# Kernel tuning notes

Measured on AMD Instinct MI355X. Metric: run time of the kernel, lower is better.

Reference implementation:

```python
import jax, jax.numpy as jnp
import numpy as np

U1, U2 = 128, 32  # GRU units


def gru(x, kernel, rec_kernel, bias, act, rec_act):
    """Keras GRU with reset_after=True. x: [B,T,F], kernel: [F,3U],
    rec_kernel: [U,3U], bias: [2,3U] (input bias, recurrent bias).
    Gate order is [z, r, h]. Returns (sequence [B,T,U], last state [B,U])."""
    B = x.shape[0]
    U = rec_kernel.shape[0]
    # Precompute the input projection for all timesteps in one big matmul.
    xb = jnp.einsum('btf,fg->btg', x, kernel) + bias[0]  # [B,T,3U]

    def step(h, xt):
        inner = h @ rec_kernel + bias[1]                 # [B,3U]
        xz, xr, xh = jnp.split(xt, 3, axis=-1)
        iz, ir, ih = jnp.split(inner, 3, axis=-1)
        z = rec_act(xz + iz)
        r = rec_act(xr + ir)
        hh = act(xh + r * ih)
        h_new = z * h + (1.0 - z) * hh
        return h_new, h_new

    h0 = jnp.zeros((B, U), x.dtype)
    hT, hs = jax.lax.scan(step, h0, jnp.swapaxes(xb, 0, 1))  # scan over T
    return jnp.swapaxes(hs, 0, 1), hT


def setup_inputs() -> dict:
    key = jax.random.key(0)
    ks = jax.random.split(key, 9)
    B, T, F = 512, 1024, 1
    s = 0.05
    return {
        'x':   jax.random.normal(ks[0], (B, T, F), jnp.float32),
        'k1':  jax.random.normal(ks[1], (F, 3 * U1), jnp.float32) * s,
        'rk1': jax.random.normal(ks[2], (U1, 3 * U1), jnp.float32) * s,
        'b1':  jnp.zeros((2, 3 * U1), jnp.float32),
        'k2':  jax.random.normal(ks[3], (U1, 3 * U2), jnp.float32) * s,
        'rk2': jax.random.normal(ks[4], (U2, 3 * U2), jnp.float32) * s,
        'b2':  jnp.zeros((2, 3 * U2), jnp.float32),
        'wd':  jax.random.normal(ks[5], (U2, 1), jnp.float32) * s,
        'bd':  jnp.zeros((1,), jnp.float32),
    }


def reference(x, k1, rk1, b1, k2, rk2, b2, wd, bd):
    # GRU-1: activation=tanh, recurrent_activation=relu, return_sequences=True
    seq1, _ = gru(x, k1, rk1, b1, jnp.tanh, jax.nn.relu)
    # Dropout(0.5) is identity at inference time.
    # GRU-2: activation=relu, recurrent_activation=sigmoid, return last state
    _, h2 = gru(seq1, k2, rk2, b2, jax.nn.relu, jax.nn.sigmoid)
    return h2 @ wd + bd  # [B,1]
```

## Files before the change

### kernel.cpp

```cpp
#include <hip/hip_runtime.h>
#include <math.h>

#define TT 1024
#define U1 128
#define U2 32
#define NCOL 480
#define NCP 240
#define NUQ 4

typedef float f2 __attribute__((ext_vector_type(2)));

#define PK_LO(acc, w, h) asm("v_pk_fma_f32 %0, %1, %2, %0 op_sel:[0,0,0] op_sel_hi:[1,0,1]" \
                             : "+v"(acc) : "v"(w), "v"(h))
#define PK_HI(acc, w, h) asm("v_pk_fma_f32 %0, %1, %2, %0 op_sel:[0,1,0] op_sel_hi:[1,1,1]" \
                             : "+v"(acc) : "v"(w), "v"(h))

__device__ __forceinline__ float fast_tanh(float v) {
    float e = __expf(2.f * v);
    return 1.f - 2.f / (e + 1.f);
}
__device__ __forceinline__ float fast_sig(float v) {
    return 1.f / (1.f + __expf(-v));
}

__global__ __launch_bounds__(1024)
void gru_stack_kernel(const float* __restrict__ x,
                      const float* __restrict__ k1,
                      const float* __restrict__ rk1,
                      const float* __restrict__ b1,
                      const float* __restrict__ k2,
                      const float* __restrict__ rk2,
                      const float* __restrict__ b2,
                      const float* __restrict__ wd,
                      const float* __restrict__ bd,
                      float* __restrict__ out)
{
    __shared__ __align__(16) float h1s[2][U1];
    __shared__ __align__(16) float h2s[2][U2];
    __shared__ __align__(16) float part1[2][NUQ][NCOL];
    __shared__ __align__(16) float part2[2][96];
    __shared__ __align__(16) float xs[2][TT];

    const int t  = threadIdx.x;
    const int b0 = blockIdx.x * 2;

    if (t < 2 * U1) ((float*)h1s)[t] = 0.f;
    if (t < 2 * U2) ((float*)h2s)[t] = 0.f;
    for (int idx = t; idx < 2 * TT; idx += 1024)
        ((float*)xs)[idx] = x[b0 * TT + idx];

    f2 w2[32];
    const float4* pb0 = nullptr;
    const float4* pb1 = nullptr;
    float2* pd0 = nullptr;
    float2* pd1 = nullptr;
    const bool is_dot = (t < 1008);
    if (t < 960) {
        const int uq = t / NCP, p = t % NCP;
        const int c0 = 2 * p, ub = 32 * uq;
#pragma unroll
        for (int j = 0; j < 32; ++j) {
            const int u = ub + j;
            float vv[2];
#pragma unroll
            for (int r = 0; r < 2; ++r) {
                const int c = c0 + r;
                vv[r] = (c < 384) ? rk1[u * 384 + c] : k2[u * 96 + (c - 384)];
            }
            w2[j].x = vv[0]; w2[j].y = vv[1];
        }
        pb0 = (const float4*)&h1s[0][ub];
        pb1 = (const float4*)&h1s[1][ub];
        pd0 = (float2*)&part1[0][uq][c0];
        pd1 = (float2*)&part1[1][uq][c0];
    } else if (t < 1008) {
        const int q2 = t - 960, c0 = 2 * q2;
#pragma unroll
        for (int j = 0; j < 32; ++j) {
            w2[j].x = rk2[j * 96 + c0 + 0];
            w2[j].y = rk2[j * 96 + c0 + 1];
        }
        pb0 = (const float4*)&h2s[0][0];
        pb1 = (const float4*)&h2s[1][0];
        pd0 = (float2*)&part2[0][c0];
        pd1 = (float2*)&part2[1][c0];
    } else {
#pragma unroll
        for (int j = 0; j < 32; ++j) { w2[j].x = 0.f; w2[j].y = 0.f; }
    }

    const int ju = t & 127, bu = t >> 7;
    float k1z = 0, k1r = 0, k1h = 0, bz = 0, br = 0, bhx = 0, bhr = 0, h_old = 0;
    if (t < 256) {
        k1z = k1[ju]; k1r = k1[128 + ju]; k1h = k1[256 + ju];
        bz  = b1[ju]       + b1[384 + ju];
        br  = b1[128 + ju] + b1[384 + 128 + ju];
        bhx = b1[256 + ju];
        bhr = b1[384 + 256 + ju];
    }
    const int tau = t - 256, j2 = tau & 31, bb2 = tau >> 5;
    float bz2 = 0, br2 = 0, bh2x = 0, bh2r = 0, h2_old = 0;
    if (t >= 256 && t < 320) {
        bz2  = b2[j2]      + b2[96 + j2];
        br2  = b2[32 + j2] + b2[96 + 32 + j2];
        bh2x = b2[64 + j2];
        bh2r = b2[96 + 64 + j2];
    }

    __syncthreads();

    for (int i = 0; i <= TT; ++i) {
        if (is_dot) {
            f2 a0 = {0.f, 0.f};
            f2 a1 = {0.f, 0.f};
#pragma unroll
            for (int k = 0; k < 8; ++k) {
                const float4 h0 = pb0[k];
                const float4 h1 = pb1[k];
                const f2 h0lo = {h0.x, h0.y}, h0hi = {h0.z, h0.w};
                const f2 h1lo = {h1.x, h1.y}, h1hi = {h1.z, h1.w};
                PK_LO(a0, w2[4 * k],     h0lo);
                PK_HI(a0, w2[4 * k + 1], h0lo);
                PK_LO(a0, w2[4 * k + 2], h0hi);
                PK_HI(a0, w2[4 * k + 3], h0hi);
                PK_LO(a1, w2[4 * k],     h1lo);
                PK_HI(a1, w2[4 * k + 1], h1lo);
                PK_LO(a1, w2[4 * k + 2], h1hi);
                PK_HI(a1, w2[4 * k + 3], h1hi);
            }
            *pd0 = make_float2(a0.x, a0.y);
            *pd1 = make_float2(a1.x, a1.y);
        }
        __syncthreads();

        if (t < 256 && i < TT) {
            const float xv = xs[bu][i];
            float iz = part1[bu][0][ju] + part1[bu][1][ju]
                     + part1[bu][2][ju] + part1[bu][3][ju];
            float ir = part1[bu][0][128 + ju] + part1[bu][1][128 + ju]
                     + part1[bu][2][128 + ju] + part1[bu][3][128 + ju];
            float ih = part1[bu][0][256 + ju] + part1[bu][1][256 + ju]
                     + part1[bu][2][256 + ju] + part1[bu][3][256 + ju];
            float z  = fmaxf(fmaf(xv, k1z, bz) + iz, 0.f);
            float r  = fmaxf(fmaf(xv, k1r, br) + ir, 0.f);
            float hh = fast_tanh(fmaf(xv, k1h, bhx) + r * (ih + bhr));
            h_old = fmaf(z, h_old - hh, hh);
            h1s[bu][ju] = h_old;
        } else if (t >= 256 && t < 320 && i >= 1) {
            float xz = part1[bb2][0][384 + j2] + part1[bb2][1][384 + j2]
                     + part1[bb2][2][384 + j2] + part1[bb2][3][384 + j2];
            float xr = part1[bb2][0][416 + j2] + part1[bb2][1][416 + j2]
                     + part1[bb2][2][416 + j2] + part1[bb2][3][416 + j2];
            float xh = part1[bb2][0][448 + j2] + part1[bb2][1][448 + j2]
                     + part1[bb2][2][448 + j2] + part1[bb2][3][448 + j2];
            float iz = part2[bb2][j2];
            float ir = part2[bb2][32 + j2];
            float ih = part2[bb2][64 + j2];
            float z  = fast_sig(xz + iz + bz2);
            float r  = fast_sig(xr + ir + br2);
            float hh = fmaxf(xh + bh2x + r * (ih + bh2r), 0.f);
            h2_old = fmaf(z, h2_old - hh, hh);
            h2s[bb2][j2] = h2_old;
        }
        __syncthreads();
    }

    if (t < 64) {
        const int b = t >> 5, j = t & 31;
        float p = h2s[b][j] * wd[j];
#pragma unroll
        for (int m = 16; m >= 1; m >>= 1) p += __shfl_xor(p, m, 64);
        if (j == 0) out[b0 + b] = p + bd[0];
    }
}

extern "C" void kernel_launch(void* const* d_in, const int* in_sizes, int n_in,
                              void* d_out, int out_size, void* d_ws, size_t ws_size,
                              hipStream_t stream) {
    const float* x   = (const float*)d_in[0];
    const float* k1  = (const float*)d_in[1];
    const float* rk1 = (const float*)d_in[2];
    const float* b1  = (const float*)d_in[3];
    const float* k2  = (const float*)d_in[4];
    const float* rk2 = (const float*)d_in[5];
    const float* b2  = (const float*)d_in[6];
    const float* wd  = (const float*)d_in[7];
    const float* bd  = (const float*)d_in[8];
    float* out = (float*)d_out;

    dim3 grid(256), block(1024);
    hipLaunchKernelGGL(gru_stack_kernel, grid, block, 0, stream,
                       x, k1, rk1, b1, k2, rk2, b2, wd, bd, out);
}
```

Baseline: 1.178 ms.

## Broadcast hidden state via readlane into SGPRs instead of LDS float4 loads

Each wave now loads one hidden-state element per lane from LDS and broadcasts it with v_readlane into scalar registers that feed packed FMAs. This replaces repeated per-thread float4 LDS reads of the shared hidden vector. The thread-to-column mapping is reorganised by wave: the rk2 recurrent dot product is folded into the spare lanes of the fourth wave of each unit quarter, and the gate-update threads are remapped to whole waves. The change adds many readlane instructions and an extra rk2 loop executed by every 'heavy' wave.

```diff
diff --git a/kernel.cpp b/kernel.cpp
--- a/kernel.cpp
+++ b/kernel.cpp
@@ -4,16 +4,14 @@
 #define TT 1024
 #define U1 128
 #define U2 32
-#define NCOL 480
-#define NCP 240
-#define NUQ 4
+#define PCOL 512
 
 typedef float f2 __attribute__((ext_vector_type(2)));
 
-#define PK_LO(acc, w, h) asm("v_pk_fma_f32 %0, %1, %2, %0 op_sel:[0,0,0] op_sel_hi:[1,0,1]" \
-                             : "+v"(acc) : "v"(w), "v"(h))
-#define PK_HI(acc, w, h) asm("v_pk_fma_f32 %0, %1, %2, %0 op_sel:[0,1,0] op_sel_hi:[1,1,1]" \
-                             : "+v"(acc) : "v"(w), "v"(h))
+#define PKS_LO(acc, w, hs) asm("v_pk_fma_f32 %0, %1, %2, %0 op_sel:[0,0,0] op_sel_hi:[1,0,1]" \
+                               : "+v"(acc) : "v"(w), "s"(hs))
+#define PKS_HI(acc, w, hs) asm("v_pk_fma_f32 %0, %1, %2, %0 op_sel:[0,1,0] op_sel_hi:[1,1,1]" \
+                               : "+v"(acc) : "v"(w), "s"(hs))
 
 __device__ __forceinline__ float fast_tanh(float v) {
     float e = __expf(2.f * v);
@@ -21,6 +19,9 @@
 }
 __device__ __forceinline__ float fast_sig(float v) {
     return 1.f / (1.f + __expf(-v));
+}
+__device__ __forceinline__ float rlf(float v, int l) {
+    return __int_as_float(__builtin_amdgcn_readlane(__float_as_int(v), l));
 }
 
 __global__ __launch_bounds__(1024)
@@ -37,70 +38,62 @@
 {
     __shared__ __align__(16) float h1s[2][U1];
     __shared__ __align__(16) float h2s[2][U2];
-    __shared__ __align__(16) float part1[2][NUQ][NCOL];
+    __shared__ __align__(16) float part1[2][4][PCOL];
     __shared__ __align__(16) float part2[2][96];
     __shared__ __align__(16) float xs[2][TT];
 
-    const int t  = threadIdx.x;
-    const int b0 = blockIdx.x * 2;
+    const int t    = threadIdx.x;
+    const int b0   = blockIdx.x * 2;
+    const int w    = t >> 6, lane = t & 63;
+    const int uq   = w >> 2, ub = 32 * uq;
+    const int pi   = ((w & 3) << 6) + lane;
+    const bool heavy = ((w & 3) == 3);
+    const int sp   = uq * 16 + (lane - 48);
+    const bool isRk2 = heavy && (lane >= 48) && (sp < 48);
+    const int c0   = 2 * pi;
+    const int c0r  = 2 * sp;
 
-    if (t < 2 * U1) ((float*)h1s)[t] = 0.f;
-    if (t < 2 * U2) ((float*)h2s)[t] = 0.f;
+    if (t < 256) ((float*)h1s)[t] = 0.f;
+    if (t < 64)  ((float*)h2s)[t] = 0.f;
     for (int idx = t; idx < 2 * TT; idx += 1024)
         ((float*)xs)[idx] = x[b0 * TT + idx];
 
     f2 w2[32];
-    const float4* pb0 = nullptr;
-    const float4* pb1 = nullptr;
-    float2* pd0 = nullptr;
-    float2* pd1 = nullptr;
-    const bool is_dot = (t < 1008);
-    if (t < 960) {
-        const int uq = t / NCP, p = t % NCP;
-        const int c0 = 2 * p, ub = 32 * uq;
+    if (pi < 240) {
 #pragma unroll
         for (int j = 0; j < 32; ++j) {
             const int u = ub + j;
-            float vv[2];
-#pragma unroll
-            for (int r = 0; r < 2; ++r) {
-                const int c = c0 + r;
-                vv[r] = (c < 384) ? rk1[u * 384 + c] : k2[u * 96 + (c - 384)];
-            }
-            w2[j].x = vv[0]; w2[j].y = vv[1];
+            const int c1 = c0 + 1;
+            const float v0 = (c0 < 384) ? rk1[u * 384 + c0] : k2[u * 96 + (c0 - 384)];
+            const float v1 = (c1 < 384) ? rk1[u * 384 + c1] : k2[u * 96 + (c1 - 384)];
+            w2[j].x = v0; w2[j].y = v1;
         }
-        pb0 = (const float4*)&h1s[0][ub];
-        pb1 = (const float4*)&h1s[1][ub];
-        pd0 = (float2*)&part1[0][uq][c0];
-        pd1 = (float2*)&part1[1][uq][c0];
-    } else if (t < 1008) {
-        const int q2 = t - 960, c0 = 2 * q2;
+    } else if (isRk2) {
 #pragma unroll
         for (int j = 0; j < 32; ++j) {
-            w2[j].x = rk2[j * 96 + c0 + 0];
-            w2[j].y = rk2[j * 96 + c0 + 1];
+            w2[j].x = rk2[j * 96 + c0r];
+            w2[j].y = rk2[j * 96 + c0r + 1];
         }
-        pb0 = (const float4*)&h2s[0][0];
-        pb1 = (const float4*)&h2s[1][0];
-        pd0 = (float2*)&part2[0][c0];
-        pd1 = (float2*)&part2[1][c0];
     } else {
 #pragma unroll
         for (int j = 0; j < 32; ++j) { w2[j].x = 0.f; w2[j].y = 0.f; }
     }
 
-    const int ju = t & 127, bu = t >> 7;
+    const bool isU1 = (w < 2) || (w == 4) || (w == 5);
+    const int bu = (w >= 4) ? 1 : 0;
+    const int ju = (w < 2) ? t : (t - 256);
     float k1z = 0, k1r = 0, k1h = 0, bz = 0, br = 0, bhx = 0, bhr = 0, h_old = 0;
-    if (t < 256) {
+    if (isU1) {
         k1z = k1[ju]; k1r = k1[128 + ju]; k1h = k1[256 + ju];
         bz  = b1[ju]       + b1[384 + ju];
         br  = b1[128 + ju] + b1[384 + 128 + ju];
         bhx = b1[256 + ju];
         bhr = b1[384 + 256 + ju];
     }
-    const int tau = t - 256, j2 = tau & 31, bb2 = tau >> 5;
+    const bool isU2 = (w == 8);
+    const int tau = t - 512, j2 = tau & 31, bb2 = (tau >> 5) & 1;
     float bz2 = 0, br2 = 0, bh2x = 0, bh2r = 0, h2_old = 0;
-    if (t >= 256 && t < 320) {
+    if (isU2) {
         bz2  = b2[j2]      + b2[96 + j2];
         br2  = b2[32 + j2] + b2[96 + 32 + j2];
         bh2x = b2[64 + j2];
@@ -110,30 +103,40 @@
     __syncthreads();
 
     for (int i = 0; i <= TT; ++i) {
-        if (is_dot) {
-            f2 a0 = {0.f, 0.f};
-            f2 a1 = {0.f, 0.f};
+        const float hv = ((const float*)h1s)[((lane >> 5) << 7) + ub + (lane & 31)];
+        f2 a0 = {0.f, 0.f}, a1 = {0.f, 0.f};
 #pragma unroll
-            for (int k = 0; k < 8; ++k) {
-                const float4 h0 = pb0[k];
-                const float4 h1 = pb1[k];
-                const f2 h0lo = {h0.x, h0.y}, h0hi = {h0.z, h0.w};
-                const f2 h1lo = {h1.x, h1.y}, h1hi = {h1.z, h1.w};
-                PK_LO(a0, w2[4 * k],     h0lo);
-                PK_HI(a0, w2[4 * k + 1], h0lo);
-                PK_LO(a0, w2[4 * k + 2], h0hi);
-                PK_HI(a0, w2[4 * k + 3], h0hi);
-                PK_LO(a1, w2[4 * k],     h1lo);
-                PK_HI(a1, w2[4 * k + 1], h1lo);
-                PK_LO(a1, w2[4 * k + 2], h1hi);
-                PK_HI(a1, w2[4 * k + 3], h1hi);
+        for (int jj = 0; jj < 16; ++jj) {
+            const f2 hs0 = { rlf(hv, 2 * jj),      rlf(hv, 2 * jj + 1) };
+            const f2 hs1 = { rlf(hv, 32 + 2 * jj), rlf(hv, 32 + 2 * jj + 1) };
+            PKS_LO(a0, w2[2 * jj],     hs0);
+            PKS_HI(a0, w2[2 * jj + 1], hs0);
+            PKS_LO(a1, w2[2 * jj],     hs1);
+            PKS_HI(a1, w2[2 * jj + 1], hs1);
+        }
+        *(float2*)&part1[0][uq][c0] = make_float2(a0.x, a0.y);
+        *(float2*)&part1[1][uq][c0] = make_float2(a1.x, a1.y);
+
+        if (heavy) {
+            const float hv2 = ((const float*)h2s)[((lane >> 5) << 5) + (lane & 31)];
+            f2 r0 = {0.f, 0.f}, r1 = {0.f, 0.f};
+#pragma unroll
+            for (int jj = 0; jj < 16; ++jj) {
+                const f2 gs0 = { rlf(hv2, 2 * jj),      rlf(hv2, 2 * jj + 1) };
+                const f2 gs1 = { rlf(hv2, 32 + 2 * jj), rlf(hv2, 32 + 2 * jj + 1) };
+                PKS_LO(r0, w2[2 * jj],     gs0);
+                PKS_HI(r0, w2[2 * jj + 1], gs0);
+                PKS_LO(r1, w2[2 * jj],     gs1);
+                PKS_HI(r1, w2[2 * jj + 1], gs1);
             }
-            *pd0 = make_float2(a0.x, a0.y);
-            *pd1 = make_float2(a1.x, a1.y);
+            if ((lane >= 48) && (sp < 48)) {
+                *(float2*)&part2[0][c0r] = make_float2(r0.x, r0.y);
+                *(float2*)&part2[1][c0r] = make_float2(r1.x, r1.y);
+            }
         }
         __syncthreads();
 
-        if (t < 256 && i < TT) {
+        if (isU1 && i < TT) {
             const float xv = xs[bu][i];
             float iz = part1[bu][0][ju] + part1[bu][1][ju]
                      + part1[bu][2][ju] + part1[bu][3][ju];
@@ -146,7 +149,7 @@
             float hh = fast_tanh(fmaf(xv, k1h, bhx) + r * (ih + bhr));
             h_old = fmaf(z, h_old - hh, hh);
             h1s[bu][ju] = h_old;
-        } else if (t >= 256 && t < 320 && i >= 1) {
+        } else if (isU2 && i >= 1) {
             float xz = part1[bb2][0][384 + j2] + part1[bb2][1][384 + j2]
                      + part1[bb2][2][384 + j2] + part1[bb2][3][384 + j2];
             float xr = part1[bb2][0][416 + j2] + part1[bb2][1][416 + j2]
```

Result: slower. 2.400 ms (+103.6%).
